# Performance work log

Measured on AMD Instinct MI355X. Metric: run time of the kernel, lower is better.

## Reference

```python
import jax, jax.numpy as jnp
import numpy as np

B, D, DOUT, R, H = 16384, 1024, 1024, 8, 16
DH = D // 2  # route hidden dim


def setup_inputs() -> dict:
    key = jax.random.key(0)
    ks = jax.random.split(key, 12)
    s = 0.02
    return {
        "x": jax.random.normal(ks[0], (B, D), dtype=jnp.float32),
        # nn.MultiheadAttention packed in_proj: [3D, D] (q,k,v stacked)
        "in_proj_w": jax.random.normal(ks[1], (3 * D, D), dtype=jnp.float32) * s,
        "in_proj_b": jax.random.normal(ks[2], (3 * D,), dtype=jnp.float32) * s,
        "out_proj_w": jax.random.normal(ks[3], (D, D), dtype=jnp.float32) * s,
        "out_proj_b": jax.random.normal(ks[4], (D,), dtype=jnp.float32) * s,
        # R expert MLPs, batched: Linear(D, D//2) -> ReLU -> Linear(D//2, DOUT)
        "W1": jax.random.normal(ks[5], (R, DH, D), dtype=jnp.float32) * s,
        "b1": jax.random.normal(ks[6], (R, DH), dtype=jnp.float32) * s,
        "W2": jax.random.normal(ks[7], (R, DOUT, DH), dtype=jnp.float32) * s,
        "b2": jax.random.normal(ks[8], (R, DOUT), dtype=jnp.float32) * s,
        # gate: Linear(D, R) + softmax
        "Wg": jax.random.normal(ks[9], (R, D), dtype=jnp.float32) * s,
        "bg": jax.random.normal(ks[10], (R,), dtype=jnp.float32) * s,
    }


def reference(x, in_proj_w, in_proj_b, out_proj_w, out_proj_b, W1, b1, W2, b2, Wg, bg):
    # --- MultiheadAttention over seq_len == 1 ---
    # softmax over a single key position is exactly 1 (for every head),
    # so attn_output == V; the Q/K projections provably do not affect the
    # output or any gradient (d softmax(single logit) = 0). Hence only the
    # V slice of the packed in_proj and the output projection matter.
    Wv = in_proj_w[2 * D:]          # [D, D]
    bv = in_proj_b[2 * D:]          # [D]
    v = x @ Wv.T + bv               # [B, D]
    attended = v @ out_proj_w.T + out_proj_b  # [B, D]

    # --- R small expert MLPs as one batched/grouped GEMM (dropout in eval mode = identity) ---
    h = jax.nn.relu(jnp.einsum('bd,rhd->brh', attended, W1) + b1)   # [B, R, DH]
    route_out = jnp.einsum('brh,roh->bro', h, W2) + b2              # [B, R, DOUT]

    # --- softmax gate over routes, computed from the ORIGINAL x ---
    gate = jax.nn.softmax(x @ Wg.T + bg, axis=-1)                   # [B, R]

    # gate-weighted sum over routes
    return jnp.einsum('bro,br->bo', route_out, gate)                # [B, DOUT]
```

## Files before the change

kernel.cpp:

```cpp
#include <hip/hip_runtime.h>
#include <hip/hip_bf16.h>
#include <cstdint>

typedef __hip_bfloat16 bf16;
typedef __attribute__((ext_vector_type(8))) short bfrag;
typedef __attribute__((ext_vector_type(4))) float facc;

#define B_    16384
#define D_    1024
#define DOUT_ 1024
#define R_    8
#define DH_   512
#define RH_   4096

#define BM 256
#define BN 256
#define BK 64

#define NXCD 8

#define AS1(p) ((const __attribute__((address_space(1))) void*)(p))
#define AS3(p) ((__attribute__((address_space(3))) void*)(p))

#define DSR(dst, addr, off) \
    asm volatile("ds_read_b128 %0, %1 offset:%c2" : "=v"(dst) : "v"(addr), "i"(off))
#define LGKM(n) do { asm volatile("s_waitcnt lgkmcnt(" #n ")" ::: "memory"); \
                     __builtin_amdgcn_sched_barrier(0); } while (0)

static __device__ __forceinline__ uint32_t pack2bf(float a, float b) {
    unsigned short ua = __builtin_bit_cast(unsigned short, __float2bfloat16(a));
    unsigned short ub = __builtin_bit_cast(unsigned short, __float2bfloat16(b));
    return (uint32_t)ua | ((uint32_t)ub << 16);
}

__global__ void k_cvt(const float* __restrict__ in, bf16* __restrict__ out, long n)
{
    long i = ((long)blockIdx.x * blockDim.x + threadIdx.x) * 4;
    if (i >= n) return;
    float4 v = *reinterpret_cast<const float4*>(in + i);
    uint2 o;
    o.x = pack2bf(v.x, v.y);
    o.y = pack2bf(v.z, v.w);
    *reinterpret_cast<uint2*>(out + i) = o;
}

__global__ void k_cvt_w2(const float* __restrict__ W2, bf16* __restrict__ out)
{
    int b = blockIdx.x;
    int r = b >> 10;
    int o = b & 1023;
    const float4* src = reinterpret_cast<const float4*>(W2 + ((long)r * DOUT_ + o) * DH_);
    bf16* dst = out + (long)o * RH_ + r * DH_;
    int t = threadIdx.x;
    float4 v = src[t];
    uint2 p;
    p.x = pack2bf(v.x, v.y);
    p.y = pack2bf(v.z, v.w);
    *reinterpret_cast<uint2*>(dst + t * 4) = p;
}

__global__ __launch_bounds__(256) void k_gate(const float* __restrict__ x,
                                              const float* __restrict__ Wg,
                                              const float* __restrict__ bg,
                                              float* __restrict__ gate)
{
    __shared__ float sWg[R_ * D_];
    __shared__ float sbg[R_];
    for (int i = threadIdx.x; i < R_ * D_ / 4; i += 256)
        reinterpret_cast<float4*>(sWg)[i] = reinterpret_cast<const float4*>(Wg)[i];
    if (threadIdx.x < R_) sbg[threadIdx.x] = bg[threadIdx.x];
    __syncthreads();

    const int lane = threadIdx.x & 63;
    const int wave = threadIdx.x >> 6;
    const int row  = blockIdx.x * 4 + wave;

    const float4* xr = reinterpret_cast<const float4*>(x + (long)row * D_);
    float s[R_] = {};
    #pragma unroll
    for (int c = 0; c < 4; ++c) {
        float4 xv = xr[lane + c * 64];
        #pragma unroll
        for (int r = 0; r < R_; ++r) {
            float4 wv = reinterpret_cast<const float4*>(sWg + r * D_)[lane + c * 64];
            s[r] += xv.x * wv.x + xv.y * wv.y + xv.z * wv.z + xv.w * wv.w;
        }
    }
    #pragma unroll
    for (int r = 0; r < R_; ++r) {
        float v = s[r];
        #pragma unroll
        for (int off = 32; off > 0; off >>= 1) v += __shfl_xor(v, off);
        s[r] = v + sbg[r];
    }
    float m = s[0];
    #pragma unroll
    for (int r = 1; r < R_; ++r) m = fmaxf(m, s[r]);
    float den = 0.f;
    #pragma unroll
    for (int r = 0; r < R_; ++r) { s[r] = __expf(s[r] - m); den += s[r]; }
    float inv = 1.f / den;
    if (lane < R_) gate[(long)row * R_ + lane] = s[lane] * inv;
}

#define MFMA_BF16 __builtin_amdgcn_mfma_f32_16x16x32_bf16

template <int EPI>
__global__ __launch_bounds__(512, 2)
void k_gemm(const bf16* __restrict__ A, const bf16* __restrict__ Bm,
            const float* __restrict__ bias, const float* __restrict__ gate,
            const float* __restrict__ b2v, void* __restrict__ Cout,
            int M, int N, int K, int gate_row0)
{
    __shared__ char lds[131072];

    const int tid  = threadIdx.x;
    const int lane = tid & 63;
    const int wave = tid >> 6;
    const int wr   = wave >> 2;
    const int wc   = wave & 3;

    const int nwg  = gridDim.x * gridDim.y;
    const int orig = blockIdx.y * gridDim.x + blockIdx.x;
    const int xcd  = orig % NXCD;
    const int q    = nwg / NXCD;
    const int rr   = nwg % NXCD;
    const int wgid = (xcd < rr ? xcd * (q + 1) : rr * (q + 1) + (xcd - rr) * q)
                   + orig / NXCD;
    const int bn0  = (wgid % gridDim.x) * BN;
    const int bm0  = (wgid / gridDim.x) * BM;

    const int lrow = lane & 15;
    const int kgrp = lane >> 4;

    const int s_colb  = ((tid & 7) * 16) ^ (((tid >> 3) & 7) << 4);
    const int s_row   = tid >> 3;
    const int lds_off = tid * 16;

    const long Kb   = (long)K * 2;
    const long r64  = 64 * Kb;
    const long r128 = 128 * Kb;
    const char* gA0 = (const char*)A  + (long)(bm0 + s_row) * Kb + s_colb;
    const char* gB0 = (const char*)Bm + (long)(bn0 + s_row) * Kb + s_colb;

    auto stageH = [&](int buf, int h, long kb) {
        char* ldst = lds + buf * 65536
                   + (h < 2 ? h * 16384 : 32768 + (h - 2) * 16384) + lds_off;
        const char* g = (h < 2 ? gA0 + h * r128 : gB0 + (h - 2) * r128) + kb;
        __builtin_amdgcn_global_load_lds(AS1(g),       AS3(ldst),        16, 0, 0);
        __builtin_amdgcn_global_load_lds(AS1(g + r64), AS3(ldst + 8192), 16, 0, 0);
    };

    const int swzk  = (lrow & 7) << 4;
    const int colK0 = (kgrp * 16) ^ swzk;
    const int colK1 = (kgrp * 16 + 64) ^ swzk;
    const uint32_t ldsbase = (uint32_t)(uintptr_t)AS3(lds);
    const uint32_t aA00 = ldsbase + (wr * 128 + lrow) * 128 + colK0;
    const uint32_t aA01 = ldsbase + (wr * 128 + lrow) * 128 + colK1;
    const uint32_t aB00 = ldsbase + 32768 + (wc * 64 + lrow) * 128 + colK0;
    const uint32_t aB01 = ldsbase + 32768 + (wc * 64 + lrow) * 128 + colK1;
    const uint32_t aA10 = aA00 + 65536, aA11 = aA01 + 65536;
    const uint32_t aB10 = aB00 + 65536, aB11 = aB01 + 65536;

    facc acc[8][4];
    #pragma unroll
    for (int m = 0; m < 8; ++m)
        #pragma unroll
        for (int n = 0; n < 4; ++n)
            acc[m][n] = facc{0.f, 0.f, 0.f, 0.f};

    const int NT = K / BK;

    bfrag aF[4][2];
    bfrag bHi[2][2];
    bfrag bLoE[2][2];
    bfrag bLoO[2][2];

    auto rdQ0 = [&](bfrag (&bLo)[2][2], uint32_t A0, uint32_t A1,
                    uint32_t B0, uint32_t B1) {
        DSR(bLo[0][0], B0, 0);    DSR(bLo[0][1], B1, 0);
        DSR(bLo[1][0], B0, 2048); DSR(bLo[1][1], B1, 2048);
        #pragma unroll
        for (int m = 0; m < 4; ++m) {
            DSR(aF[m][0], A0, m * 2048);
            DSR(aF[m][1], A1, m * 2048);
        }
    };

    stageH(0, 0, 0); stageH(0, 1, 0); stageH(0, 2, 0); stageH(0, 3, 0);
    stageH(1, 0, 128); stageH(1, 1, 128);
    asm volatile("s_waitcnt vmcnt(4)" ::: "memory");
    __builtin_amdgcn_s_barrier();
    rdQ0(bLoE, aA00, aA01, aB00, aB01);

    auto ktile = [&](int t, int curbuf,
                     uint32_t A0c, uint32_t A1c, uint32_t B0c, uint32_t B1c,
                     uint32_t A0n, uint32_t A1n, uint32_t B0n, uint32_t B1n,
                     bfrag (&bLoC)[2][2], bfrag (&bLoN)[2][2]) {
        const long k1b = (long)(t + 1) * 128;
        const long k2b = (long)(t + 2) * 128;
        const int  nb  = curbuf ^ 1;

        if (t + 1 < NT) stageH(nb, 2, k1b);
        __builtin_amdgcn_s_barrier();
        __builtin_amdgcn_s_setprio(1);
        LGKM(6);
        acc[0][0] = MFMA_BF16(aF[0][0], bLoC[0][0], acc[0][0], 0, 0, 0);
        acc[0][0] = MFMA_BF16(aF[0][1], bLoC[0][1], acc[0][0], 0, 0, 0);
        acc[0][1] = MFMA_BF16(aF[0][0], bLoC[1][0], acc[0][1], 0, 0, 0);
        acc[0][1] = MFMA_BF16(aF[0][1], bLoC[1][1], acc[0][1], 0, 0, 0);
        LGKM(4);
        acc[1][0] = MFMA_BF16(aF[1][0], bLoC[0][0], acc[1][0], 0, 0, 0);
        acc[1][0] = MFMA_BF16(aF[1][1], bLoC[0][1], acc[1][0], 0, 0, 0);
        acc[1][1] = MFMA_BF16(aF[1][0], bLoC[1][0], acc[1][1], 0, 0, 0);
        acc[1][1] = MFMA_BF16(aF[1][1], bLoC[1][1], acc[1][1], 0, 0, 0);
        LGKM(2);
        acc[2][0] = MFMA_BF16(aF[2][0], bLoC[0][0], acc[2][0], 0, 0, 0);
        acc[2][0] = MFMA_BF16(aF[2][1], bLoC[0][1], acc[2][0], 0, 0, 0);
        acc[2][1] = MFMA_BF16(aF[2][0], bLoC[1][0], acc[2][1], 0, 0, 0);
        acc[2][1] = MFMA_BF16(aF[2][1], bLoC[1][1], acc[2][1], 0, 0, 0);
        LGKM(0);
        acc[3][0] = MFMA_BF16(aF[3][0], bLoC[0][0], acc[3][0], 0, 0, 0);
        acc[3][0] = MFMA_BF16(aF[3][1], bLoC[0][1], acc[3][0], 0, 0, 0);
        acc[3][1] = MFMA_BF16(aF[3][0], bLoC[1][0], acc[3][1], 0, 0, 0);
        acc[3][1] = MFMA_BF16(aF[3][1], bLoC[1][1], acc[3][1], 0, 0, 0);
        __builtin_amdgcn_s_setprio(0);
        DSR(bHi[0][0], B0c, 2 * 2048); DSR(bHi[0][1], B1c, 2 * 2048);
        DSR(bHi[1][0], B0c, 3 * 2048); DSR(bHi[1][1], B1c, 3 * 2048);
        __builtin_amdgcn_s_barrier();

        if (t + 1 < NT) stageH(nb, 3, k1b);
        __builtin_amdgcn_s_barrier();
        __builtin_amdgcn_s_setprio(1);
        LGKM(2);
        #pragma unroll
        for (int m = 0; m < 4; ++m) {
            acc[m][2] = MFMA_BF16(aF[m][0], bHi[0][0], acc[m][2], 0, 0, 0);
            acc[m][2] = MFMA_BF16(aF[m][1], bHi[0][1], acc[m][2], 0, 0, 0);
        }
        LGKM(0);
        #pragma unroll
        for (int m = 0; m < 4; ++m) {
            acc[m][3] = MFMA_BF16(aF[m][0], bHi[1][0], acc[m][3], 0, 0, 0);
            acc[m][3] = MFMA_BF16(aF[m][1], bHi[1][1], acc[m][3], 0, 0, 0);
        }
        __builtin_amdgcn_s_setprio(0);
        #pragma unroll
        for (int m = 0; m < 4; ++m) {
            DSR(aF[m][0], A0c, (4 + m) * 2048);
            DSR(aF[m][1], A1c, (4 + m) * 2048);
        }
        __builtin_amdgcn_s_barrier();

        if (t + 2 < NT) stageH(curbuf, 0, k2b);
        __builtin_amdgcn_s_barrier();
        __builtin_amdgcn_s_setprio(1);
        LGKM(6);
        acc[4][2] = MFMA_BF16(aF[0][0], bHi[0][0], acc[4][2], 0, 0, 0);
        acc[4][2] = MFMA_BF16(aF[0][1], bHi[0][1], acc[4][2], 0, 0, 0);
        acc[4][3] = MFMA_BF16(aF[0][0], bHi[1][0], acc[4][3], 0, 0, 0);
        acc[4][3] = MFMA_BF16(aF[0][1], bHi[1][1], acc[4][3], 0, 0, 0);
        LGKM(4);
        acc[5][2] = MFMA_BF16(aF[1][0], bHi[0][0], acc[5][2], 0, 0, 0);
        acc[5][2] = MFMA_BF16(aF[1][1], bHi[0][1], acc[5][2], 0, 0, 0);
        acc[5][3] = MFMA_BF16(aF[1][0], bHi[1][0], acc[5][3], 0, 0, 0);
        acc[5][3] = MFMA_BF16(aF[1][1], bHi[1][1], acc[5][3], 0, 0, 0);
        LGKM(2);
        acc[6][2] = MFMA_BF16(aF[2][0], bHi[0][0], acc[6][2], 0, 0, 0);
        acc[6][2] = MFMA_BF16(aF[2][1], bHi[0][1], acc[6][2], 0, 0, 0);
        acc[6][3] = MFMA_BF16(aF[2][0], bHi[1][0], acc[6][3], 0, 0, 0);
        acc[6][3] = MFMA_BF16(aF[2][1], bHi[1][1], acc[6][3], 0, 0, 0);
        LGKM(0);
        acc[7][2] = MFMA_BF16(aF[3][0], bHi[0][0], acc[7][2], 0, 0, 0);
        acc[7][2] = MFMA_BF16(aF[3][1], bHi[0][1], acc[7][2], 0, 0, 0);
        acc[7][3] = MFMA_BF16(aF[3][0], bHi[1][0], acc[7][3], 0, 0, 0);
        acc[7][3] = MFMA_BF16(aF[3][1], bHi[1][1], acc[7][3], 0, 0, 0);
        __builtin_amdgcn_s_setprio(0);
        __builtin_amdgcn_s_barrier();

        if (t + 2 < NT) {
            stageH(curbuf, 1, k2b);
            asm volatile("s_waitcnt vmcnt(4)" ::: "memory");
        } else if (t + 1 < NT) {
            asm volatile("s_waitcnt vmcnt(0)" ::: "memory");
        }
        __builtin_amdgcn_s_barrier();
        __builtin_amdgcn_s_setprio(1);
        #pragma unroll
        for (int m = 0; m < 4; ++m) {
            acc[4 + m][0] = MFMA_BF16(aF[m][0], bLoC[0][0], acc[4 + m][0], 0, 0, 0);
            acc[4 + m][0] = MFMA_BF16(aF[m][1], bLoC[0][1], acc[4 + m][0], 0, 0, 0);
            acc[4 + m][1] = MFMA_BF16(aF[m][0], bLoC[1][0], acc[4 + m][1], 0, 0, 0);
            acc[4 + m][1] = MFMA_BF16(aF[m][1], bLoC[1][1], acc[4 + m][1], 0, 0, 0);
        }
        __builtin_amdgcn_s_setprio(0);
        if (t + 1 < NT) rdQ0(bLoN, A0n, A1n, B0n, B1n);
        __builtin_amdgcn_s_barrier();
    };

    for (int t = 0; t < NT; t += 2) {
        ktile(t,     0, aA00, aA01, aB00, aB01, aA10, aA11, aB10, aB11, bLoE, bLoO);
        ktile(t + 1, 1, aA10, aA11, aB10, aB11, aA00, aA01, aB00, aB01, bLoO, bLoE);
    }

    if constexpr (EPI == 2) {
        float* Cf = reinterpret_cast<float*>(Cout);
        float b2c[4][R_];
        #pragma unroll
        for (int n = 0; n < 4; ++n) {
            const int col = bn0 + wc * 64 + n * 16 + lrow;
            #pragma unroll
            for (int r = 0; r < R_; ++r) b2c[n][r] = b2v[r * N + col];
        }
        #pragma unroll
        for (int m = 0; m < 8; ++m) {
            #pragma unroll
            for (int j = 0; j < 4; ++j) {
                const int row = bm0 + wr * 128 + m * 16 + kgrp * 4 + j;
                const float* g = gate + (long)(gate_row0 + row) * R_;
                float gv[R_];
                #pragma unroll
                for (int r = 0; r < R_; ++r) gv[r] = g[r];
                #pragma unroll
                for (int n = 0; n < 4; ++n) {
                    const int col = bn0 + wc * 64 + n * 16 + lrow;
                    float sv = acc[m][n][j];
                    #pragma unroll
                    for (int r = 0; r < R_; ++r) sv += gv[r] * b2c[n][r];
                    Cf[(long)row * N + col] = sv;
                }
            }
        }
    } else {
        bf16* Cb = reinterpret_cast<bf16*>(Cout);
        float bcol[4];
        #pragma unroll
        for (int n = 0; n < 4; ++n) bcol[n] = bias[bn0 + wc * 64 + n * 16 + lrow];
        #pragma unroll
        for (int m = 0; m < 8; ++m) {
            #pragma unroll
            for (int j = 0; j < 4; ++j) {
                const int row = bm0 + wr * 128 + m * 16 + kgrp * 4 + j;
                float gv[4];
                if constexpr (EPI == 1) {
                    #pragma unroll
                    for (int n = 0; n < 4; ++n) {
                        const int col = bn0 + wc * 64 + n * 16 + lrow;
                        gv[n] = gate[(long)(gate_row0 + row) * R_ + (col >> 9)];
                    }
                }
                #pragma unroll
                for (int n = 0; n < 4; ++n) {
                    const int col = bn0 + wc * 64 + n * 16 + lrow;
                    float v = acc[m][n][j] + bcol[n];
                    if constexpr (EPI == 1) v = fmaxf(v, 0.f) * gv[n];
                    Cb[(long)row * N + col] = __float2bfloat16(v);
                }
            }
        }
    }
}

extern "C" void kernel_launch(void* const* d_in, const int* in_sizes, int n_in,
                              void* d_out, int out_size, void* d_ws, size_t ws_size,
                              hipStream_t stream)
{
    const float* x   = (const float*)d_in[0];
    const float* ipw = (const float*)d_in[1];
    const float* ipb = (const float*)d_in[2];
    const float* opw = (const float*)d_in[3];
    const float* opb = (const float*)d_in[4];
    const float* W1  = (const float*)d_in[5];
    const float* b1  = (const float*)d_in[6];
    const float* W2  = (const float*)d_in[7];
    const float* b2  = (const float*)d_in[8];
    const float* Wg  = (const float*)d_in[9];
    const float* bg  = (const float*)d_in[10];
    float* out = (float*)d_out;

    char* ws = (char*)d_ws;
    size_t off = 0;
    auto alloc = [&](size_t bytes) -> void* {
        void* p = ws + off;
        off += (bytes + 255) & ~(size_t)255;
        return p;
    };

    bf16* xb   = (bf16*)alloc((size_t)B_ * D_ * 2);
    bf16* vb   = (bf16*)alloc((size_t)B_ * D_ * 2);
    bf16* Wvb  = (bf16*)alloc((size_t)D_ * D_ * 2);
    bf16* Wob  = (bf16*)alloc((size_t)D_ * D_ * 2);
    bf16* W1b  = (bf16*)alloc((size_t)RH_ * D_ * 2);
    bf16* W2b  = (bf16*)alloc((size_t)DOUT_ * RH_ * 2);
    float* gate = (float*)alloc((size_t)B_ * R_ * 4);

    int mc = B_;
    while (off + (size_t)mc * RH_ * 2 > ws_size && mc > 1024) mc >>= 1;
    bf16* hb = (bf16*)alloc((size_t)mc * RH_ * 2);
    bf16* ab = xb;

    k_cvt<<<(B_ * D_) / 1024, 256, 0, stream>>>(x, xb, (long)B_ * D_);
    k_cvt<<<(D_ * D_) / 1024, 256, 0, stream>>>(ipw + (size_t)2 * D_ * D_, Wvb, (long)D_ * D_);
    k_cvt<<<(D_ * D_) / 1024, 256, 0, stream>>>(opw, Wob, (long)D_ * D_);
    k_cvt<<<(RH_ * D_) / 1024, 256, 0, stream>>>(W1, W1b, (long)RH_ * D_);
    k_cvt_w2<<<R_ * DOUT_, 128, 0, stream>>>(W2, W2b);

    k_gate<<<B_ / 4, 256, 0, stream>>>(x, Wg, bg, gate);

    k_gemm<0><<<dim3(D_ / BN, B_ / BM), 512, 0, stream>>>(
        xb, Wvb, ipb + 2 * D_, nullptr, nullptr, vb, B_, D_, D_, 0);

    k_gemm<0><<<dim3(D_ / BN, B_ / BM), 512, 0, stream>>>(
        vb, Wob, opb, nullptr, nullptr, ab, B_, D_, D_, 0);

    for (int m0 = 0; m0 < B_; m0 += mc) {
        k_gemm<1><<<dim3(RH_ / BN, mc / BM), 512, 0, stream>>>(
            ab + (size_t)m0 * D_, W1b, b1, gate, nullptr, hb, mc, RH_, D_, m0);
        k_gemm<2><<<dim3(DOUT_ / BN, mc / BM), 512, 0, stream>>>(
            hb, W2b, nullptr, gate, b2, out + (size_t)m0 * DOUT_, mc, DOUT_, RH_, m0);
    }
}
```

Baseline: 377.3 us.

## Fold V and output projections into one precomputed effective weight

Since attended = (x Wv^T + bv) Wo^T + bo, the two chained B×D×D GEMMs are replaced by one weight-space GEMM that computes Weff = Wo·Wv (a D×D×D product, using a transposed bf16 copy of Wv) and an effective bias beff = Wo·bv + bo. A single B×D×D GEMM then applies Weff to x. This removes one large activation GEMM and the intermediate v buffer, at the cost of a small weight GEMM, a transpose kernel and a bias reduction each call. Weff is rounded to bf16, which changes the rounding behaviour compared with two separately rounded GEMMs.

After: 381.8 us. About the same (+1.2%).

```diff
diff --git a/kernel.cpp b/kernel.cpp
--- a/kernel.cpp
+++ b/kernel.cpp
@@ -57,6 +57,50 @@
     p.x = pack2bf(v.x, v.y);
     p.y = pack2bf(v.z, v.w);
     *reinterpret_cast<uint2*>(dst + t * 4) = p;
+}
+
+__global__ __launch_bounds__(256) void k_cvt_wvT(const float* __restrict__ Wv,
+                                                 bf16* __restrict__ outT)
+{
+    __shared__ float tile[64][65];
+    const int j0 = blockIdx.y * 64;
+    const int d0 = blockIdx.x * 64;
+    const int tx = threadIdx.x & 15;
+    const int ty = threadIdx.x >> 4;
+    #pragma unroll
+    for (int p = 0; p < 4; ++p) {
+        int r = p * 16 + ty;
+        float4 v = *reinterpret_cast<const float4*>(&Wv[(long)(j0 + r) * D_ + d0 + tx * 4]);
+        tile[r][tx * 4 + 0] = v.x; tile[r][tx * 4 + 1] = v.y;
+        tile[r][tx * 4 + 2] = v.z; tile[r][tx * 4 + 3] = v.w;
+    }
+    __syncthreads();
+    #pragma unroll
+    for (int p = 0; p < 4; ++p) {
+        int r = p * 16 + ty;
+        uint2 o;
+        o.x = pack2bf(tile[tx * 4 + 0][r], tile[tx * 4 + 1][r]);
+        o.y = pack2bf(tile[tx * 4 + 2][r], tile[tx * 4 + 3][r]);
+        *reinterpret_cast<uint2*>(&outT[(long)(d0 + r) * D_ + j0 + tx * 4]) = o;
+    }
+}
+
+__global__ __launch_bounds__(256) void k_beff(const float* __restrict__ Wout,
+                                              const float* __restrict__ bv,
+                                              const float* __restrict__ bout,
+                                              float* __restrict__ beff)
+{
+    const int o = blockIdx.x;
+    float s = 0.f;
+    for (int d = threadIdx.x; d < D_; d += 256)
+        s += Wout[(long)o * D_ + d] * bv[d];
+    #pragma unroll
+    for (int off = 32; off > 0; off >>= 1) s += __shfl_xor(s, off);
+    __shared__ float ps[4];
+    if ((threadIdx.x & 63) == 0) ps[threadIdx.x >> 6] = s;
+    __syncthreads();
+    if (threadIdx.x == 0)
+        beff[o] = ps[0] + ps[1] + ps[2] + ps[3] + bout[o];
 }
 
 __global__ __launch_bounds__(256) void k_gate(const float* __restrict__ x,
@@ -335,7 +379,10 @@
         bf16* Cb = reinterpret_cast<bf16*>(Cout);
         float bcol[4];
         #pragma unroll
-        for (int n = 0; n < 4; ++n) bcol[n] = bias[bn0 + wc * 64 + n * 16 + lrow];
+        for (int n = 0; n < 4; ++n) {
+            if constexpr (EPI == 3) bcol[n] = 0.f;
+            else bcol[n] = bias[bn0 + wc * 64 + n * 16 + lrow];
+        }
         #pragma unroll
         for (int m = 0; m < 8; ++m) {
             #pragma unroll
@@ -378,6 +425,9 @@
     const float* bg  = (const float*)d_in[10];
     float* out = (float*)d_out;
 
+    const float* Wv_f = ipw + (size_t)2 * D_ * D_;
+    const float* bv_f = ipb + 2 * D_;
+
     char* ws = (char*)d_ws;
     size_t off = 0;
     auto alloc = [&](size_t bytes) -> void* {
@@ -387,9 +437,11 @@
     };
 
     bf16* xb   = (bf16*)alloc((size_t)B_ * D_ * 2);
-    bf16* vb   = (bf16*)alloc((size_t)B_ * D_ * 2);
-    bf16* Wvb  = (bf16*)alloc((size_t)D_ * D_ * 2);
+    bf16* ab   = (bf16*)alloc((size_t)B_ * D_ * 2);
     bf16* Wob  = (bf16*)alloc((size_t)D_ * D_ * 2);
+    bf16* WvT  = (bf16*)alloc((size_t)D_ * D_ * 2);
+    bf16* Weff = (bf16*)alloc((size_t)D_ * D_ * 2);
+    float* beff = (float*)alloc((size_t)D_ * 4);
     bf16* W1b  = (bf16*)alloc((size_t)RH_ * D_ * 2);
     bf16* W2b  = (bf16*)alloc((size_t)DOUT_ * RH_ * 2);
     float* gate = (float*)alloc((size_t)B_ * R_ * 4);
@@ -397,21 +449,21 @@
     int mc = B_;
     while (off + (size_t)mc * RH_ * 2 > ws_size && mc > 1024) mc >>= 1;
     bf16* hb = (bf16*)alloc((size_t)mc * RH_ * 2);
-    bf16* ab = xb;
 
     k_cvt<<<(B_ * D_) / 1024, 256, 0, stream>>>(x, xb, (long)B_ * D_);
-    k_cvt<<<(D_ * D_) / 1024, 256, 0, stream>>>(ipw + (size_t)2 * D_ * D_, Wvb, (long)D_ * D_);
     k_cvt<<<(D_ * D_) / 1024, 256, 0, stream>>>(opw, Wob, (long)D_ * D_);
+    k_cvt_wvT<<<dim3(16, 16), 256, 0, stream>>>(Wv_f, WvT);
     k_cvt<<<(RH_ * D_) / 1024, 256, 0, stream>>>(W1, W1b, (long)RH_ * D_);
     k_cvt_w2<<<R_ * DOUT_, 128, 0, stream>>>(W2, W2b);
+    k_beff<<<D_, 256, 0, stream>>>(opw, bv_f, opb, beff);
 
     k_gate<<<B_ / 4, 256, 0, stream>>>(x, Wg, bg, gate);
 
+    k_gemm<3><<<dim3(D_ / BN, D_ / BM), 512, 0, stream>>>(
+        Wob, WvT, nullptr, nullptr, nullptr, Weff, D_, D_, D_, 0);
+
     k_gemm<0><<<dim3(D_ / BN, B_ / BM), 512, 0, stream>>>(
-        xb, Wvb, ipb + 2 * D_, nullptr, nullptr, vb, B_, D_, D_, 0);
-
-    k_gemm<0><<<dim3(D_ / BN, B_ / BM), 512, 0, stream>>>(
-        vb, Wob, opb, nullptr, nullptr, ab, B_, D_, D_, 0);
+        xb, Weff, beff, nullptr, nullptr, ab, B_, D_, D_, 0);
 
     for (int m0 = 0; m0 < B_; m0 += mc) {
         k_gemm<1><<<dim3(RH_ / BN, mc / BM), 512, 0, stream>>>(
```
